# Performance work log

Hardware: AMD Instinct MI355X
Metric: run time of the kernel (lower is better)

## Reference

```python
import jax, jax.numpy as jnp
import numpy as np

N, E, H, L, G = 50000, 800000, 128, 4, 64

def setup_inputs() -> dict:
    key = jax.random.key(0)
    ks = jax.random.split(key, 16)
    s = 0.05
    x = jax.random.normal(ks[0], (N, H), jnp.float32)
    edge_index = jax.random.randint(ks[1], (2, E), 0, N)
    edge_attr = jax.random.normal(ks[2], (E, 1), jnp.float32)
    # sorted graph assignment covering all G graphs (batch[-1]+1 == G)
    batch = (jnp.arange(N) * G) // N
    conv_W1 = jax.random.normal(ks[3], (L, H, H), jnp.float32) * s
    conv_b1 = jnp.zeros((L, H), jnp.float32)
    conv_W2 = jax.random.normal(ks[4], (L, H, H), jnp.float32) * s
    conv_b2 = jnp.zeros((L, H), jnp.float32)
    conv_eps = jnp.zeros((L,), jnp.float32)  # torch init: eps = 0
    edge_W = jax.random.normal(ks[5], (L, 1, H), jnp.float32) * s
    edge_b = jnp.zeros((L, H), jnp.float32)
    vn_W1 = jax.random.normal(ks[6], (L - 1, H, H), jnp.float32) * s
    vn_b1 = jnp.zeros((L - 1, H), jnp.float32)
    vn_W2 = jax.random.normal(ks[7], (L - 1, H, H), jnp.float32) * s
    vn_b2 = jnp.zeros((L - 1, H), jnp.float32)
    vn_emb = jnp.zeros((H,), jnp.float32)  # torch init: constant 0
    return dict(x=x, edge_attr=edge_attr, conv_W1=conv_W1, conv_b1=conv_b1,
                conv_W2=conv_W2, conv_b2=conv_b2, conv_eps=conv_eps,
                edge_W=edge_W, edge_b=edge_b, vn_W1=vn_W1, vn_b1=vn_b1,
                vn_W2=vn_W2, vn_b2=vn_b2, vn_emb=vn_emb,
                edge_index=edge_index, batch=batch)


def reference(x, edge_attr, conv_W1, conv_b1, conv_W2, conv_b2, conv_eps,
              edge_W, edge_b, vn_W1, vn_b1, vn_W2, vn_b2, vn_emb,
              edge_index, batch):
    src, tgt = edge_index[0], edge_index[1]
    # PyG mean aggregation: divide scatter-sum by in-degree (clamped to 1)
    deg = jnp.maximum(
        jax.ops.segment_sum(jnp.ones((E,), x.dtype), tgt, num_segments=N), 1.0)[:, None]
    vn = jnp.broadcast_to(vn_emb[None, :], (G, H))  # virtual node per graph
    h = x
    hs = []
    for i in range(L):
        h = h + vn[batch]
        edge_emb = edge_attr @ edge_W[i] + edge_b[i]          # [E,H]
        msg = jax.nn.relu(h[src] + edge_emb)                   # gather + relu
        agg = jax.ops.segment_sum(msg, tgt, num_segments=N) / deg  # mean scatter
        z = (1.0 + conv_eps[i]) * h + agg
        h = jax.nn.relu(z @ conv_W1[i] + conv_b1[i]) @ conv_W2[i] + conv_b2[i]
        hs.append(h)
        if i < L - 1:
            vt = jax.ops.segment_sum(hs[i], batch, num_segments=G) + vn
            vn = jax.nn.relu(
                jax.nn.relu(vt @ vn_W1[i] + vn_b1[i]) @ vn_W2[i] + vn_b2[i])
            # eval mode: dropout is identity
    return jnp.concatenate(hs, axis=1)  # [N, L*H] jumping-knowledge concat
```

## Files before the change

### kernel.cpp

```cpp
#include <hip/hip_runtime.h>

#define NN 50000
#define EE 800000
#define HH 128
#define LL 4
#define GG 64
#define NR 50048

typedef short bf16x8 __attribute__((ext_vector_type(8)));
typedef float f32x4 __attribute__((ext_vector_type(4)));

__device__ __forceinline__ unsigned bf_round(float f) {
  unsigned u = __float_as_uint(f);
  return (u + 0x7fffu + ((u >> 16) & 1u)) >> 16;
}
__device__ __forceinline__ unsigned bf_pack2(float lo, float hi) {
  return bf_round(lo) | (bf_round(hi) << 16);
}

__global__ __launch_bounds__(256) void count_kernel(const int* __restrict__ tgt,
                                                    int* __restrict__ cnt, int E) {
  int e = blockIdx.x * 256 + threadIdx.x;
  if (e < E) atomicAdd(&cnt[tgt[e]], 1);
}

__global__ __launch_bounds__(256) void blocksum_kernel(const int* __restrict__ cnt,
                                                       int* __restrict__ bs, int N) {
  int i = blockIdx.x * 256 + threadIdx.x;
  int v = (i < N) ? cnt[i] : 0;
  __shared__ int sm[256];
  sm[threadIdx.x] = v;
  __syncthreads();
  for (int s = 128; s >= 1; s >>= 1) {
    if (threadIdx.x < s) sm[threadIdx.x] += sm[threadIdx.x + s];
    __syncthreads();
  }
  if (threadIdx.x == 0) bs[blockIdx.x] = sm[0];
}

__global__ __launch_bounds__(256) void bs_scan_kernel(int* __restrict__ bs, int nb) {
  __shared__ int sm[256];
  int t = threadIdx.x;
  int v = (t < nb) ? bs[t] : 0;
  sm[t] = v;
  __syncthreads();
  for (int off = 1; off < 256; off <<= 1) {
    int u = (t >= off) ? sm[t - off] : 0;
    __syncthreads();
    sm[t] += u;
    __syncthreads();
  }
  if (t < nb) bs[t] = sm[t] - v;
  if (t == 255) bs[nb] = sm[255];
}

__global__ __launch_bounds__(256) void blockscan_kernel(const int* __restrict__ cnt,
                                                        const int* __restrict__ bs,
                                                        int* __restrict__ rp,
                                                        int* __restrict__ cur, int N, int nb) {
  int b = blockIdx.x, t = threadIdx.x;
  int i = b * 256 + t;
  int v = (i < N) ? cnt[i] : 0;
  __shared__ int sm[256];
  sm[t] = v;
  __syncthreads();
  for (int off = 1; off < 256; off <<= 1) {
    int u = (t >= off) ? sm[t - off] : 0;
    __syncthreads();
    sm[t] += u;
    __syncthreads();
  }
  if (i < N) { rp[i] = sm[t] - v + bs[b]; cur[i] = 0; }
  if (b == 0 && t == 0) rp[N] = bs[nb];
}

__global__ __launch_bounds__(256) void scatter_kernel(const int* __restrict__ src,
                                                      const int* __restrict__ tgt,
                                                      const float* __restrict__ attr,
                                                      const int* __restrict__ rp,
                                                      int* __restrict__ cur,
                                                      int2* __restrict__ es, int E) {
  int e = blockIdx.x * 256 + threadIdx.x;
  if (e < E) {
    int t = tgt[e];
    int p = rp[t] + atomicAdd(&cur[t], 1);
    int2 rec;
    rec.x = src[e];
    rec.y = __float_as_int(attr[e]);
    es[p] = rec;
  }
}

__global__ __launch_bounds__(256) void init_kernel(const float* __restrict__ W1,
                                                   const float* __restrict__ W2,
                                                   const float* __restrict__ emb,
                                                   short* __restrict__ wt1,
                                                   short* __restrict__ wt2,
                                                   float* __restrict__ vn,
                                                   float* __restrict__ part) {
  int idx = blockIdx.x * 256 + threadIdx.x;
  const int NW = 2 * LL * HH * HH;
  if (idx < NW) {
    int m = idx >> 14;
    int r = idx & 16383;
    int n = r >> 7, k = r & 127;
    const float* W = (m < LL) ? (W1 + (size_t)m * 16384) : (W2 + (size_t)(m - LL) * 16384);
    short* D = (m < LL) ? (wt1 + (size_t)m * 16384) : (wt2 + (size_t)(m - LL) * 16384);
    D[n * 128 + k] = (short)bf_round(W[k * 128 + n]);
  } else if (idx < NW + GG * HH) {
    int i = idx - NW;
    vn[i] = emb[i & (HH - 1)];
  } else if (idx < NW + 2 * GG * HH) {
    part[idx - NW - GG * HH] = 0.f;
  }
}

__global__ __launch_bounds__(256) void pack_kernel(const float4* __restrict__ hp, int pitch4,
                                                   const float4* __restrict__ vn,
                                                   const float4* __restrict__ ebias,
                                                   const int* __restrict__ batch,
                                                   uint2* __restrict__ hbf, int N) {
  int idx = blockIdx.x * 256 + threadIdx.x;
  if (idx >= N * (HH / 4)) return;
  int n = idx >> 5;
  int c4 = idx & 31;
  int g = batch[n];
  float4 a = hp[(size_t)n * pitch4 + c4];
  float4 b = vn[g * 32 + c4];
  float4 e = ebias[c4];
  uint2 o;
  o.x = bf_pack2(a.x + b.x + e.x, a.y + b.y + e.y);
  o.y = bf_pack2(a.z + b.z + e.z, a.w + b.w + e.w);
  hbf[idx] = o;
}

__device__ __forceinline__ void accum8s(float* acc, uint4 p, float a, float m,
                                        const float4& ew0, const float4& ew1) {
  acc[0] = fmaf(m, fmaxf(fmaf(a, ew0.x, __uint_as_float(p.x << 16)), 0.f), acc[0]);
  acc[1] = fmaf(m, fmaxf(fmaf(a, ew0.y, __uint_as_float(p.x & 0xffff0000u)), 0.f), acc[1]);
  acc[2] = fmaf(m, fmaxf(fmaf(a, ew0.z, __uint_as_float(p.y << 16)), 0.f), acc[2]);
  acc[3] = fmaf(m, fmaxf(fmaf(a, ew0.w, __uint_as_float(p.y & 0xffff0000u)), 0.f), acc[3]);
  acc[4] = fmaf(m, fmaxf(fmaf(a, ew1.x, __uint_as_float(p.z << 16)), 0.f), acc[4]);
  acc[5] = fmaf(m, fmaxf(fmaf(a, ew1.y, __uint_as_float(p.z & 0xffff0000u)), 0.f), acc[5]);
  acc[6] = fmaf(m, fmaxf(fmaf(a, ew1.z, __uint_as_float(p.w << 16)), 0.f), acc[6]);
  acc[7] = fmaf(m, fmaxf(fmaf(a, ew1.w, __uint_as_float(p.w & 0xffff0000u)), 0.f), acc[7]);
}

__global__ __launch_bounds__(128) void agg_kernel(const uint4* __restrict__ hbf4,
                                                  const float* __restrict__ hp, int pitch,
                                                  const float* __restrict__ vnp,
                                                  const int* __restrict__ batch,
                                                  const int2* __restrict__ es,
                                                  const int* __restrict__ rp,
                                                  const float* __restrict__ eW,
                                                  const float* __restrict__ epsp,
                                                  uint4* __restrict__ zb4, int N) {
  int wave = threadIdx.x >> 6;
  int lane = threadIdx.x & 63;
  int n = blockIdx.x * 2 + wave;
  if (n >= N) return;
  int q = lane >> 4;
  int c = lane & 15;
  float4 ew0 = *(const float4*)(eW + c * 8);
  float4 ew1 = *(const float4*)(eW + c * 8 + 4);
  int rs = rp[n], re = rp[n + 1];
  int cnt = re - rs;
  float acc[8];
#pragma unroll
  for (int j = 0; j < 8; ++j) acc[j] = 0.f;
  for (int k = 0; k < cnt; k += 16) {
    int i0 = rs + min(k + q, cnt - 1);
    int i1 = rs + min(k + 4 + q, cnt - 1);
    int i2 = rs + min(k + 8 + q, cnt - 1);
    int i3 = rs + min(k + 12 + q, cnt - 1);
    int2 e0 = es[i0];
    int2 e1 = es[i1];
    int2 e2 = es[i2];
    int2 e3 = es[i3];
    uint4 p0 = hbf4[(size_t)e0.x * 16 + c];
    uint4 p1 = hbf4[(size_t)e1.x * 16 + c];
    uint4 p2 = hbf4[(size_t)e2.x * 16 + c];
    uint4 p3 = hbf4[(size_t)e3.x * 16 + c];
    float m0 = (k + q < cnt) ? 1.f : 0.f;
    float m1 = (k + 4 + q < cnt) ? 1.f : 0.f;
    float m2 = (k + 8 + q < cnt) ? 1.f : 0.f;
    float m3 = (k + 12 + q < cnt) ? 1.f : 0.f;
    accum8s(acc, p0, __int_as_float(e0.y), m0, ew0, ew1);
    accum8s(acc, p1, __int_as_float(e1.y), m1, ew0, ew1);
    accum8s(acc, p2, __int_as_float(e2.y), m2, ew0, ew1);
    accum8s(acc, p3, __int_as_float(e3.y), m3, ew0, ew1);
  }
#pragma unroll
  for (int j = 0; j < 8; ++j) {
    acc[j] += __shfl_xor(acc[j], 16);
    acc[j] += __shfl_xor(acc[j], 32);
  }
  int g = batch[n];
  const float* hrow = hp + (size_t)n * pitch + c * 8;
  const float* vrow = vnp + g * HH + c * 8;
  float4 h0 = *(const float4*)(hrow);
  float4 h1 = *(const float4*)(hrow + 4);
  float4 v0 = *(const float4*)(vrow);
  float4 v1 = *(const float4*)(vrow + 4);
  float inv = 1.f / fmaxf((float)cnt, 1.f);
  float onep = 1.f + epsp[0];
  uint4 o;
  o.x = bf_pack2(fmaf(onep, h0.x + v0.x, acc[0] * inv),
                 fmaf(onep, h0.y + v0.y, acc[1] * inv));
  o.y = bf_pack2(fmaf(onep, h0.z + v0.z, acc[2] * inv),
                 fmaf(onep, h0.w + v0.w, acc[3] * inv));
  o.z = bf_pack2(fmaf(onep, h1.x + v1.x, acc[4] * inv),
                 fmaf(onep, h1.y + v1.y, acc[5] * inv));
  o.w = bf_pack2(fmaf(onep, h1.z + v1.z, acc[6] * inv),
                 fmaf(onep, h1.w + v1.w, acc[7] * inv));
  if (q == 0) zb4[(size_t)n * 16 + c] = o;
}

__global__ __launch_bounds__(256) void mlp_kernel(const unsigned* __restrict__ zb,
                                                  const short* __restrict__ wt1,
                                                  const float* __restrict__ b1,
                                                  const short* __restrict__ wt2,
                                                  const float* __restrict__ b2,
                                                  float* __restrict__ out,
                                                  float* __restrict__ part,
                                                  int do_gs, int layer, int N) {
  __shared__ char smem[64 * 272];
  int tid = threadIdx.x;
  int w = tid >> 6, lane = tid & 63;
  int l15 = lane & 15, q = lane >> 4;
  int row0 = blockIdx.x * 64;
  int wrow = w * 16;

  const uint4* z4 = (const uint4*)zb;
#pragma unroll
  for (int it = 0; it < 4; ++it) {
    int f = lane + it * 64;
    int r = f >> 4, c16 = f & 15;
    uint4 v = z4[(size_t)(row0 + wrow + r) * 16 + c16];
    *(uint4*)(&smem[(wrow + r) * 272 + c16 * 16]) = v;
  }

  f32x4 zero = {0.f, 0.f, 0.f, 0.f};
  f32x4 acc[8];
#pragma unroll
  for (int j = 0; j < 8; ++j) acc[j] = zero;

#pragma unroll
  for (int s = 0; s < 4; ++s) {
    bf16x8 af = *(const bf16x8*)(&smem[(wrow + l15) * 272 + (s * 32 + q * 8) * 2]);
#pragma unroll
    for (int j = 0; j < 8; ++j) {
      bf16x8 bf = *(const bf16x8*)(wt1 + (size_t)(j * 16 + l15) * 128 + s * 32 + q * 8);
      acc[j] = __builtin_amdgcn_mfma_f32_16x16x32_bf16(af, bf, acc[j], 0, 0, 0);
    }
  }
#pragma unroll
  for (int j = 0; j < 8; ++j) {
    float bv = b1[j * 16 + l15];
#pragma unroll
    for (int r = 0; r < 4; ++r) {
      float v = fmaxf(acc[j][r] + bv, 0.f);
      *(short*)(&smem[(wrow + q * 4 + r) * 272 + (j * 16 + l15) * 2]) = (short)bf_round(v);
    }
    acc[j] = zero;
  }
#pragma unroll
  for (int s = 0; s < 4; ++s) {
    bf16x8 af = *(const bf16x8*)(&smem[(wrow + l15) * 272 + (s * 32 + q * 8) * 2]);
#pragma unroll
    for (int j = 0; j < 8; ++j) {
      bf16x8 bf = *(const bf16x8*)(wt2 + (size_t)(j * 16 + l15) * 128 + s * 32 + q * 8);
      acc[j] = __builtin_amdgcn_mfma_f32_16x16x32_bf16(af, bf, acc[j], 0, 0, 0);
    }
  }
  int g0 = (int)(((long long)row0 * GG) / NN);
#pragma unroll
  for (int j = 0; j < 8; ++j) {
    float bv = b2[j * 16 + l15];
    float s0 = 0.f, s1 = 0.f;
#pragma unroll
    for (int r = 0; r < 4; ++r) {
      int row = row0 + wrow + q * 4 + r;
      if (row < N) {
        float v = acc[j][r] + bv;
        out[(size_t)row * (LL * HH) + layer * HH + j * 16 + l15] = v;
        if (do_gs) {
          int rel = (int)(((long long)row * GG) / NN) - g0;
          if (rel == 0) s0 += v; else s1 += v;
        }
      }
    }
    if (do_gs) {
      s0 += __shfl_xor(s0, 16); s0 += __shfl_xor(s0, 32);
      s1 += __shfl_xor(s1, 16); s1 += __shfl_xor(s1, 32);
      if (q == 0) {
        atomicAdd(&part[g0 * HH + j * 16 + l15], s0);
        if (s1 != 0.f) atomicAdd(&part[(g0 + 1) * HH + j * 16 + l15], s1);
      }
    }
  }
}

__global__ __launch_bounds__(128) void vn_fused_kernel(float* __restrict__ part,
                                                       const float* __restrict__ W1,
                                                       const float* __restrict__ b1,
                                                       const float* __restrict__ W2,
                                                       const float* __restrict__ b2,
                                                       float* __restrict__ vn, int G) {
  int g = blockIdx.x, j = threadIdx.x;
  __shared__ float vr[128];
  __shared__ float tr[128];
  vr[j] = vn[g * HH + j] + part[g * HH + j];
  part[g * HH + j] = 0.f;
  __syncthreads();
  float a = b1[j];
  for (int k = 0; k < 128; ++k) a = fmaf(vr[k], W1[k * HH + j], a);
  tr[j] = fmaxf(a, 0.f);
  __syncthreads();
  float o = b2[j];
  for (int k = 0; k < 128; ++k) o = fmaf(tr[k], W2[k * HH + j], o);
  vn[g * HH + j] = fmaxf(o, 0.f);
}

extern "C" void kernel_launch(void* const* d_in, const int* in_sizes, int n_in,
                              void* d_out, int out_size, void* d_ws, size_t ws_size,
                              hipStream_t stream) {
  const int N = NN, E = EE, H = HH, L = LL, G = GG;
  const float* x          = (const float*)d_in[0];
  const float* edge_attr  = (const float*)d_in[1];
  const float* conv_W1    = (const float*)d_in[2];
  const float* conv_b1    = (const float*)d_in[3];
  const float* conv_W2    = (const float*)d_in[4];
  const float* conv_b2    = (const float*)d_in[5];
  const float* conv_eps   = (const float*)d_in[6];
  const float* edge_W     = (const float*)d_in[7];
  const float* edge_b     = (const float*)d_in[8];
  const float* vn_W1      = (const float*)d_in[9];
  const float* vn_b1      = (const float*)d_in[10];
  const float* vn_W2      = (const float*)d_in[11];
  const float* vn_b2      = (const float*)d_in[12];
  const float* vn_emb     = (const float*)d_in[13];
  const int*   edge_index = (const int*)d_in[14];
  const int*   batch      = (const int*)d_in[15];
  float* out = (float*)d_out;

  const int nb = (N + 255) / 256;

  char* ws = (char*)d_ws;
  size_t off = 0;
  auto take = [&](size_t bytes) -> void* {
    void* p = ws + off;
    off = (off + bytes + 255) & ~(size_t)255;
    return p;
  };
  int*      cnt  = (int*)take((size_t)N * 4);
  int*      cur  = (int*)take((size_t)N * 4);
  int*      rp   = (int*)take((size_t)(N + 1) * 4);
  int*      bs   = (int*)take((size_t)(nb + 1) * 4);
  int2*     es   = (int2*)take((size_t)E * 8);
  unsigned* hbf  = (unsigned*)take((size_t)N * (H / 2) * 4);
  unsigned* zb   = (unsigned*)take((size_t)NR * (H / 2) * 4);
  short*    wt1  = (short*)take((size_t)L * H * H * 2);
  short*    wt2  = (short*)take((size_t)L * H * H * 2);
  float*    part = (float*)take((size_t)G * H * 4);
  float*    vn   = (float*)take((size_t)G * H * 4);

  const int* src = edge_index;
  const int* tgt = edge_index + E;

  hipMemsetAsync(cnt, 0, (size_t)N * 4, stream);
  count_kernel<<<(E + 255) / 256, 256, 0, stream>>>(tgt, cnt, E);
  blocksum_kernel<<<nb, 256, 0, stream>>>(cnt, bs, N);
  bs_scan_kernel<<<1, 256, 0, stream>>>(bs, nb);
  blockscan_kernel<<<nb, 256, 0, stream>>>(cnt, bs, rp, cur, N, nb);
  scatter_kernel<<<(E + 255) / 256, 256, 0, stream>>>(src, tgt, edge_attr, rp, cur, es, E);
  init_kernel<<<(2 * L * H * H + 2 * G * H + 255) / 256, 256, 0, stream>>>(
      conv_W1, conv_W2, vn_emb, wt1, wt2, vn, part);

  for (int i = 0; i < L; ++i) {
    const float* hp;
    int pitch;
    if (i == 0) { hp = x; pitch = H; }
    else        { hp = out + (size_t)(i - 1) * H; pitch = L * H; }
    pack_kernel<<<(N * (H / 4) + 255) / 256, 256, 0, stream>>>(
        (const float4*)hp, pitch / 4, (const float4*)vn,
        (const float4*)(edge_b + (size_t)i * H), batch, (uint2*)hbf, N);
    agg_kernel<<<(N + 1) / 2, 128, 0, stream>>>(
        (const uint4*)hbf, hp, pitch, vn, batch, es, rp,
        edge_W + (size_t)i * H, conv_eps + i, (uint4*)zb, N);
    mlp_kernel<<<NR / 64, 256, 0, stream>>>(
        zb, wt1 + (size_t)i * H * H, conv_b1 + (size_t)i * H,
        wt2 + (size_t)i * H * H, conv_b2 + (size_t)i * H, out, part,
        (i < L - 1) ? 1 : 0, i, N);
    if (i < L - 1) {
      vn_fused_kernel<<<G, 128, 0, stream>>>(part, vn_W1 + (size_t)i * H * H,
                                             vn_b1 + (size_t)i * H,
                                             vn_W2 + (size_t)i * H * H,
                                             vn_b2 + (size_t)i * H, vn, G);
    }
  }
}
```

Before: 625.6 us.

## Fuse neighbor aggregation into the MLP kernel via shared memory

Merges the per-node gather/mean aggregation kernel into the MLP kernel. Each wave now aggregates its 16 rows one after another and writes the bf16 z rows straight into shared memory, replacing the global zb buffer. This removes a kernel launch and the global write and re-read of z. The cost is far fewer waves in flight for the latency-bound gather (one wave handles 16 nodes serially instead of one node per wave), which may hurt memory-latency hiding.

```diff
diff --git a/kernel.cpp b/kernel.cpp
--- a/kernel.cpp
+++ b/kernel.cpp
@@ -146,84 +146,21 @@
   acc[7] = fmaf(m, fmaxf(fmaf(a, ew1.w, __uint_as_float(p.w & 0xffff0000u)), 0.f), acc[7]);
 }
 
-__global__ __launch_bounds__(128) void agg_kernel(const uint4* __restrict__ hbf4,
-                                                  const float* __restrict__ hp, int pitch,
-                                                  const float* __restrict__ vnp,
-                                                  const int* __restrict__ batch,
-                                                  const int2* __restrict__ es,
-                                                  const int* __restrict__ rp,
-                                                  const float* __restrict__ eW,
-                                                  const float* __restrict__ epsp,
-                                                  uint4* __restrict__ zb4, int N) {
-  int wave = threadIdx.x >> 6;
-  int lane = threadIdx.x & 63;
-  int n = blockIdx.x * 2 + wave;
-  if (n >= N) return;
-  int q = lane >> 4;
-  int c = lane & 15;
-  float4 ew0 = *(const float4*)(eW + c * 8);
-  float4 ew1 = *(const float4*)(eW + c * 8 + 4);
-  int rs = rp[n], re = rp[n + 1];
-  int cnt = re - rs;
-  float acc[8];
-#pragma unroll
-  for (int j = 0; j < 8; ++j) acc[j] = 0.f;
-  for (int k = 0; k < cnt; k += 16) {
-    int i0 = rs + min(k + q, cnt - 1);
-    int i1 = rs + min(k + 4 + q, cnt - 1);
-    int i2 = rs + min(k + 8 + q, cnt - 1);
-    int i3 = rs + min(k + 12 + q, cnt - 1);
-    int2 e0 = es[i0];
-    int2 e1 = es[i1];
-    int2 e2 = es[i2];
-    int2 e3 = es[i3];
-    uint4 p0 = hbf4[(size_t)e0.x * 16 + c];
-    uint4 p1 = hbf4[(size_t)e1.x * 16 + c];
-    uint4 p2 = hbf4[(size_t)e2.x * 16 + c];
-    uint4 p3 = hbf4[(size_t)e3.x * 16 + c];
-    float m0 = (k + q < cnt) ? 1.f : 0.f;
-    float m1 = (k + 4 + q < cnt) ? 1.f : 0.f;
-    float m2 = (k + 8 + q < cnt) ? 1.f : 0.f;
-    float m3 = (k + 12 + q < cnt) ? 1.f : 0.f;
-    accum8s(acc, p0, __int_as_float(e0.y), m0, ew0, ew1);
-    accum8s(acc, p1, __int_as_float(e1.y), m1, ew0, ew1);
-    accum8s(acc, p2, __int_as_float(e2.y), m2, ew0, ew1);
-    accum8s(acc, p3, __int_as_float(e3.y), m3, ew0, ew1);
-  }
-#pragma unroll
-  for (int j = 0; j < 8; ++j) {
-    acc[j] += __shfl_xor(acc[j], 16);
-    acc[j] += __shfl_xor(acc[j], 32);
-  }
-  int g = batch[n];
-  const float* hrow = hp + (size_t)n * pitch + c * 8;
-  const float* vrow = vnp + g * HH + c * 8;
-  float4 h0 = *(const float4*)(hrow);
-  float4 h1 = *(const float4*)(hrow + 4);
-  float4 v0 = *(const float4*)(vrow);
-  float4 v1 = *(const float4*)(vrow + 4);
-  float inv = 1.f / fmaxf((float)cnt, 1.f);
-  float onep = 1.f + epsp[0];
-  uint4 o;
-  o.x = bf_pack2(fmaf(onep, h0.x + v0.x, acc[0] * inv),
-                 fmaf(onep, h0.y + v0.y, acc[1] * inv));
-  o.y = bf_pack2(fmaf(onep, h0.z + v0.z, acc[2] * inv),
-                 fmaf(onep, h0.w + v0.w, acc[3] * inv));
-  o.z = bf_pack2(fmaf(onep, h1.x + v1.x, acc[4] * inv),
-                 fmaf(onep, h1.y + v1.y, acc[5] * inv));
-  o.w = bf_pack2(fmaf(onep, h1.z + v1.z, acc[6] * inv),
-                 fmaf(onep, h1.w + v1.w, acc[7] * inv));
-  if (q == 0) zb4[(size_t)n * 16 + c] = o;
-}
-
-__global__ __launch_bounds__(256) void mlp_kernel(const unsigned* __restrict__ zb,
-                                                  const short* __restrict__ wt1,
-                                                  const float* __restrict__ b1,
-                                                  const short* __restrict__ wt2,
-                                                  const float* __restrict__ b2,
-                                                  float* __restrict__ out,
-                                                  float* __restrict__ part,
-                                                  int do_gs, int layer, int N) {
+__global__ __launch_bounds__(256) void aggmlp_kernel(const uint4* __restrict__ hbf4,
+                                                     const float* __restrict__ hp, int pitch,
+                                                     const float* __restrict__ vnp,
+                                                     const int* __restrict__ batch,
+                                                     const int2* __restrict__ es,
+                                                     const int* __restrict__ rp,
+                                                     const float* __restrict__ eW,
+                                                     const float* __restrict__ epsp,
+                                                     const short* __restrict__ wt1,
+                                                     const float* __restrict__ b1,
+                                                     const short* __restrict__ wt2,
+                                                     const float* __restrict__ b2,
+                                                     float* __restrict__ out,
+                                                     float* __restrict__ part,
+                                                     int do_gs, int layer, int N) {
   __shared__ char smem[64 * 272];
   int tid = threadIdx.x;
   int w = tid >> 6, lane = tid & 63;
@@ -231,13 +168,65 @@
   int row0 = blockIdx.x * 64;
   int wrow = w * 16;
 
-  const uint4* z4 = (const uint4*)zb;
-#pragma unroll
-  for (int it = 0; it < 4; ++it) {
-    int f = lane + it * 64;
-    int r = f >> 4, c16 = f & 15;
-    uint4 v = z4[(size_t)(row0 + wrow + r) * 16 + c16];
-    *(uint4*)(&smem[(wrow + r) * 272 + c16 * 16]) = v;
+  {
+    int c = l15;
+    float4 ew0 = *(const float4*)(eW + c * 8);
+    float4 ew1 = *(const float4*)(eW + c * 8 + 4);
+    float onep = 1.f + epsp[0];
+    for (int r = 0; r < 16; ++r) {
+      int n = row0 + wrow + r;
+      if (n >= N) break;
+      int rs = rp[n], re = rp[n + 1];
+      int cnt = re - rs;
+      float acc[8];
+#pragma unroll
+      for (int j = 0; j < 8; ++j) acc[j] = 0.f;
+      for (int k = 0; k < cnt; k += 16) {
+        int i0 = rs + min(k + q, cnt - 1);
+        int i1 = rs + min(k + 4 + q, cnt - 1);
+        int i2 = rs + min(k + 8 + q, cnt - 1);
+        int i3 = rs + min(k + 12 + q, cnt - 1);
+        int2 e0 = es[i0];
+        int2 e1 = es[i1];
+        int2 e2 = es[i2];
+        int2 e3 = es[i3];
+        uint4 p0 = hbf4[(size_t)e0.x * 16 + c];
+        uint4 p1 = hbf4[(size_t)e1.x * 16 + c];
+        uint4 p2 = hbf4[(size_t)e2.x * 16 + c];
+        uint4 p3 = hbf4[(size_t)e3.x * 16 + c];
+        float m0 = (k + q < cnt) ? 1.f : 0.f;
+        float m1 = (k + 4 + q < cnt) ? 1.f : 0.f;
+        float m2 = (k + 8 + q < cnt) ? 1.f : 0.f;
+        float m3 = (k + 12 + q < cnt) ? 1.f : 0.f;
+        accum8s(acc, p0, __int_as_float(e0.y), m0, ew0, ew1);
+        accum8s(acc, p1, __int_as_float(e1.y), m1, ew0, ew1);
+        accum8s(acc, p2, __int_as_float(e2.y), m2, ew0, ew1);
+        accum8s(acc, p3, __int_as_float(e3.y), m3, ew0, ew1);
+      }
+#pragma unroll
+      for (int j = 0; j < 8; ++j) {
+        acc[j] += __shfl_xor(acc[j], 16);
+        acc[j] += __shfl_xor(acc[j], 32);
+      }
+      int g = batch[n];
+      const float* hrow = hp + (size_t)n * pitch + c * 8;
+      const float* vrow = vnp + (size_t)g * HH + c * 8;
+      float4 h0 = *(const float4*)(hrow);
+      float4 h1 = *(const float4*)(hrow + 4);
+      float4 v0 = *(const float4*)(vrow);
+      float4 v1 = *(const float4*)(vrow + 4);
+      float inv = 1.f / fmaxf((float)cnt, 1.f);
+      uint4 o;
+      o.x = bf_pack2(fmaf(onep, h0.x + v0.x, acc[0] * inv),
+                     fmaf(onep, h0.y + v0.y, acc[1] * inv));
+      o.y = bf_pack2(fmaf(onep, h0.z + v0.z, acc[2] * inv),
+                     fmaf(onep, h0.w + v0.w, acc[3] * inv));
+      o.z = bf_pack2(fmaf(onep, h1.x + v1.x, acc[4] * inv),
+                     fmaf(onep, h1.y + v1.y, acc[5] * inv));
+      o.w = bf_pack2(fmaf(onep, h1.z + v1.z, acc[6] * inv),
+                     fmaf(onep, h1.w + v1.w, acc[7] * inv));
+      if (q == 0) *(uint4*)(&smem[(wrow + r) * 272 + c * 16]) = o;
+    }
   }
 
   f32x4 zero = {0.f, 0.f, 0.f, 0.f};
@@ -359,7 +348,6 @@
   int*      bs   = (int*)take((size_t)(nb + 1) * 4);
   int2*     es   = (int2*)take((size_t)E * 8);
   unsigned* hbf  = (unsigned*)take((size_t)N * (H / 2) * 4);
-  unsigned* zb   = (unsigned*)take((size_t)NR * (H / 2) * 4);
   short*    wt1  = (short*)take((size_t)L * H * H * 2);
   short*    wt2  = (short*)take((size_t)L * H * H * 2);
   float*    part = (float*)take((size_t)G * H * 4);
@@ -385,11 +373,10 @@
     pack_kernel<<<(N * (H / 4) + 255) / 256, 256, 0, stream>>>(
         (const float4*)hp, pitch / 4, (const float4*)vn,
         (const float4*)(edge_b + (size_t)i * H), batch, (uint2*)hbf, N);
-    agg_kernel<<<(N + 1) / 2, 128, 0, stream>>>(
+    aggmlp_kernel<<<NR / 64, 256, 0, stream>>>(
         (const uint4*)hbf, hp, pitch, vn, batch, es, rp,
-        edge_W + (size_t)i * H, conv_eps + i, (uint4*)zb, N);
-    mlp_kernel<<<NR / 64, 256, 0, stream>>>(
-        zb, wt1 + (size_t)i * H * H, conv_b1 + (size_t)i * H,
+        edge_W + (size_t)i * H, conv_eps + i,
+        wt1 + (size_t)i * H * H, conv_b1 + (size_t)i * H,
         wt2 + (size_t)i * H * H, conv_b2 + (size_t)i * H, out, part,
         (i < L - 1) ? 1 : 0, i, N);
     if (i < L - 1) {
```

New measurement: 758.6 us. +21.3%, slower.

## Fuse bf16 packing into MLP epilogue and add virtual node during aggregation

Applied to the files above, without the earlier changes.

Removes the per-layer pack kernel. The MLP kernel now writes the next layer's bf16 gather buffer (h plus the next edge bias) directly in its epilogue, and the aggregation kernel adds the per-graph virtual node vector on the fly. It gets the graph id from batch[src], packed into the upper bits of the edge record. The count and init kernels are merged into one launch. This saves a full N×H read/write pass per layer plus some launches, at the cost of extra vn loads (L2-resident) per gathered edge and 2-byte scattered stores in the MLP epilogue. Packing src into 16 bits relies on N < 65536.

```diff
diff --git a/kernel.cpp b/kernel.cpp
--- a/kernel.cpp
+++ b/kernel.cpp
@@ -18,10 +18,35 @@
   return bf_round(lo) | (bf_round(hi) << 16);
 }
 
-__global__ __launch_bounds__(256) void count_kernel(const int* __restrict__ tgt,
-                                                    int* __restrict__ cnt, int E) {
-  int e = blockIdx.x * 256 + threadIdx.x;
-  if (e < E) atomicAdd(&cnt[tgt[e]], 1);
+__global__ __launch_bounds__(256) void count_init_kernel(const int* __restrict__ tgt,
+                                                         int* __restrict__ cnt, int E, int nbE,
+                                                         const float* __restrict__ W1,
+                                                         const float* __restrict__ W2,
+                                                         const float* __restrict__ emb,
+                                                         short* __restrict__ wt1,
+                                                         short* __restrict__ wt2,
+                                                         float* __restrict__ vn,
+                                                         float* __restrict__ part) {
+  if ((int)blockIdx.x < nbE) {
+    int e = blockIdx.x * 256 + threadIdx.x;
+    if (e < E) atomicAdd(&cnt[tgt[e]], 1);
+    return;
+  }
+  int idx = (blockIdx.x - nbE) * 256 + threadIdx.x;
+  const int NW = 2 * LL * HH * HH;
+  if (idx < NW) {
+    int m = idx >> 14;
+    int r = idx & 16383;
+    int n = r >> 7, k = r & 127;
+    const float* W = (m < LL) ? (W1 + (size_t)m * 16384) : (W2 + (size_t)(m - LL) * 16384);
+    short* D = (m < LL) ? (wt1 + (size_t)m * 16384) : (wt2 + (size_t)(m - LL) * 16384);
+    D[n * 128 + k] = (short)bf_round(W[k * 128 + n]);
+  } else if (idx < NW + GG * HH) {
+    int i = idx - NW;
+    vn[i] = emb[i & (HH - 1)];
+  } else if (idx < NW + 2 * GG * HH) {
+    part[idx - NW - GG * HH] = 0.f;
+  }
 }
 
 __global__ __launch_bounds__(256) void blocksum_kernel(const int* __restrict__ cnt,
@@ -79,71 +104,50 @@
                                                       const float* __restrict__ attr,
                                                       const int* __restrict__ rp,
                                                       int* __restrict__ cur,
+                                                      const int* __restrict__ batch,
                                                       int2* __restrict__ es, int E) {
   int e = blockIdx.x * 256 + threadIdx.x;
   if (e < E) {
     int t = tgt[e];
+    int s = src[e];
     int p = rp[t] + atomicAdd(&cur[t], 1);
     int2 rec;
-    rec.x = src[e];
+    rec.x = s | (batch[s] << 16);
     rec.y = __float_as_int(attr[e]);
     es[p] = rec;
   }
 }
 
-__global__ __launch_bounds__(256) void init_kernel(const float* __restrict__ W1,
-                                                   const float* __restrict__ W2,
-                                                   const float* __restrict__ emb,
-                                                   short* __restrict__ wt1,
-                                                   short* __restrict__ wt2,
-                                                   float* __restrict__ vn,
-                                                   float* __restrict__ part) {
-  int idx = blockIdx.x * 256 + threadIdx.x;
-  const int NW = 2 * LL * HH * HH;
-  if (idx < NW) {
-    int m = idx >> 14;
-    int r = idx & 16383;
-    int n = r >> 7, k = r & 127;
-    const float* W = (m < LL) ? (W1 + (size_t)m * 16384) : (W2 + (size_t)(m - LL) * 16384);
-    short* D = (m < LL) ? (wt1 + (size_t)m * 16384) : (wt2 + (size_t)(m - LL) * 16384);
-    D[n * 128 + k] = (short)bf_round(W[k * 128 + n]);
-  } else if (idx < NW + GG * HH) {
-    int i = idx - NW;
-    vn[i] = emb[i & (HH - 1)];
-  } else if (idx < NW + 2 * GG * HH) {
-    part[idx - NW - GG * HH] = 0.f;
-  }
-}
-
-__global__ __launch_bounds__(256) void pack_kernel(const float4* __restrict__ hp, int pitch4,
-                                                   const float4* __restrict__ vn,
-                                                   const float4* __restrict__ ebias,
-                                                   const int* __restrict__ batch,
-                                                   uint2* __restrict__ hbf, int N) {
+__global__ __launch_bounds__(256) void pack0_kernel(const float4* __restrict__ xp,
+                                                    const float4* __restrict__ ebias,
+                                                    uint2* __restrict__ hbf, int N) {
   int idx = blockIdx.x * 256 + threadIdx.x;
   if (idx >= N * (HH / 4)) return;
-  int n = idx >> 5;
   int c4 = idx & 31;
-  int g = batch[n];
-  float4 a = hp[(size_t)n * pitch4 + c4];
-  float4 b = vn[g * 32 + c4];
+  float4 a = xp[idx];
   float4 e = ebias[c4];
   uint2 o;
-  o.x = bf_pack2(a.x + b.x + e.x, a.y + b.y + e.y);
-  o.y = bf_pack2(a.z + b.z + e.z, a.w + b.w + e.w);
+  o.x = bf_pack2(a.x + e.x, a.y + e.y);
+  o.y = bf_pack2(a.z + e.z, a.w + e.w);
   hbf[idx] = o;
 }
 
-__device__ __forceinline__ void accum8s(float* acc, uint4 p, float a, float m,
+__device__ __forceinline__ void accum8v(float* acc, uint4 p, float a, float m,
+                                        const float4& va, const float4& vb,
                                         const float4& ew0, const float4& ew1) {
-  acc[0] = fmaf(m, fmaxf(fmaf(a, ew0.x, __uint_as_float(p.x << 16)), 0.f), acc[0]);
-  acc[1] = fmaf(m, fmaxf(fmaf(a, ew0.y, __uint_as_float(p.x & 0xffff0000u)), 0.f), acc[1]);
-  acc[2] = fmaf(m, fmaxf(fmaf(a, ew0.z, __uint_as_float(p.y << 16)), 0.f), acc[2]);
-  acc[3] = fmaf(m, fmaxf(fmaf(a, ew0.w, __uint_as_float(p.y & 0xffff0000u)), 0.f), acc[3]);
-  acc[4] = fmaf(m, fmaxf(fmaf(a, ew1.x, __uint_as_float(p.z << 16)), 0.f), acc[4]);
-  acc[5] = fmaf(m, fmaxf(fmaf(a, ew1.y, __uint_as_float(p.z & 0xffff0000u)), 0.f), acc[5]);
-  acc[6] = fmaf(m, fmaxf(fmaf(a, ew1.z, __uint_as_float(p.w << 16)), 0.f), acc[6]);
-  acc[7] = fmaf(m, fmaxf(fmaf(a, ew1.w, __uint_as_float(p.w & 0xffff0000u)), 0.f), acc[7]);
+  float lo, hi;
+  lo = __uint_as_float(p.x << 16); hi = __uint_as_float(p.x & 0xffff0000u);
+  acc[0] = fmaf(m, fmaxf(fmaf(a, ew0.x, lo + va.x), 0.f), acc[0]);
+  acc[1] = fmaf(m, fmaxf(fmaf(a, ew0.y, hi + va.y), 0.f), acc[1]);
+  lo = __uint_as_float(p.y << 16); hi = __uint_as_float(p.y & 0xffff0000u);
+  acc[2] = fmaf(m, fmaxf(fmaf(a, ew0.z, lo + va.z), 0.f), acc[2]);
+  acc[3] = fmaf(m, fmaxf(fmaf(a, ew0.w, hi + va.w), 0.f), acc[3]);
+  lo = __uint_as_float(p.z << 16); hi = __uint_as_float(p.z & 0xffff0000u);
+  acc[4] = fmaf(m, fmaxf(fmaf(a, ew1.x, lo + vb.x), 0.f), acc[4]);
+  acc[5] = fmaf(m, fmaxf(fmaf(a, ew1.y, hi + vb.y), 0.f), acc[5]);
+  lo = __uint_as_float(p.w << 16); hi = __uint_as_float(p.w & 0xffff0000u);
+  acc[6] = fmaf(m, fmaxf(fmaf(a, ew1.z, lo + vb.z), 0.f), acc[6]);
+  acc[7] = fmaf(m, fmaxf(fmaf(a, ew1.w, hi + vb.w), 0.f), acc[7]);
 }
 
 __global__ __launch_bounds__(128) void agg_kernel(const uint4* __restrict__ hbf4,
@@ -177,18 +181,28 @@
     int2 e1 = es[i1];
     int2 e2 = es[i2];
     int2 e3 = es[i3];
-    uint4 p0 = hbf4[(size_t)e0.x * 16 + c];
-    uint4 p1 = hbf4[(size_t)e1.x * 16 + c];
-    uint4 p2 = hbf4[(size_t)e2.x * 16 + c];
-    uint4 p3 = hbf4[(size_t)e3.x * 16 + c];
+    unsigned x0 = (unsigned)e0.x, x1 = (unsigned)e1.x;
+    unsigned x2 = (unsigned)e2.x, x3 = (unsigned)e3.x;
+    uint4 p0 = hbf4[(size_t)(x0 & 0xffffu) * 16 + c];
+    uint4 p1 = hbf4[(size_t)(x1 & 0xffffu) * 16 + c];
+    uint4 p2 = hbf4[(size_t)(x2 & 0xffffu) * 16 + c];
+    uint4 p3 = hbf4[(size_t)(x3 & 0xffffu) * 16 + c];
+    const float4* vr0 = (const float4*)(vnp + (x0 >> 16) * HH + c * 8);
+    const float4* vr1 = (const float4*)(vnp + (x1 >> 16) * HH + c * 8);
+    const float4* vr2 = (const float4*)(vnp + (x2 >> 16) * HH + c * 8);
+    const float4* vr3 = (const float4*)(vnp + (x3 >> 16) * HH + c * 8);
+    float4 va0 = vr0[0], vb0 = vr0[1];
+    float4 va1 = vr1[0], vb1 = vr1[1];
+    float4 va2 = vr2[0], vb2 = vr2[1];
+    float4 va3 = vr3[0], vb3 = vr3[1];
     float m0 = (k + q < cnt) ? 1.f : 0.f;
     float m1 = (k + 4 + q < cnt) ? 1.f : 0.f;
     float m2 = (k + 8 + q < cnt) ? 1.f : 0.f;
     float m3 = (k + 12 + q < cnt) ? 1.f : 0.f;
-    accum8s(acc, p0, __int_as_float(e0.y), m0, ew0, ew1);
-    accum8s(acc, p1, __int_as_float(e1.y), m1, ew0, ew1);
-    accum8s(acc, p2, __int_as_float(e2.y), m2, ew0, ew1);
-    accum8s(acc, p3, __int_as_float(e3.y), m3, ew0, ew1);
+    accum8v(acc, p0, __int_as_float(e0.y), m0, va0, vb0, ew0, ew1);
+    accum8v(acc, p1, __int_as_float(e1.y), m1, va1, vb1, ew0, ew1);
+    accum8v(acc, p2, __int_as_float(e2.y), m2, va2, vb2, ew0, ew1);
+    accum8v(acc, p3, __int_as_float(e3.y), m3, va3, vb3, ew0, ew1);
   }
 #pragma unroll
   for (int j = 0; j < 8; ++j) {
@@ -223,7 +237,9 @@
                                                   const float* __restrict__ b2,
                                                   float* __restrict__ out,
                                                   float* __restrict__ part,
-                                                  int do_gs, int layer, int N) {
+                                                  short* __restrict__ hbfw,
+                                                  const float* __restrict__ ebn,
+                                                  int do_gs, int do_hbf, int layer, int N) {
   __shared__ char smem[64 * 272];
   int tid = threadIdx.x;
   int w = tid >> 6, lane = tid & 63;
@@ -277,6 +293,7 @@
 #pragma unroll
   for (int j = 0; j < 8; ++j) {
     float bv = b2[j * 16 + l15];
+    float ebv = do_hbf ? ebn[j * 16 + l15] : 0.f;
     float s0 = 0.f, s1 = 0.f;
 #pragma unroll
     for (int r = 0; r < 4; ++r) {
@@ -284,6 +301,8 @@
       if (row < N) {
         float v = acc[j][r] + bv;
         out[(size_t)row * (LL * HH) + layer * HH + j * 16 + l15] = v;
+        if (do_hbf)
+          hbfw[(size_t)row * HH + j * 16 + l15] = (short)bf_round(v + ebv);
         if (do_gs) {
           int rel = (int)(((long long)row * GG) / NN) - g0;
           if (rel == 0) s0 += v; else s1 += v;
@@ -345,6 +364,7 @@
   float* out = (float*)d_out;
 
   const int nb = (N + 255) / 256;
+  const int nbE = (E + 255) / 256;
 
   char* ws = (char*)d_ws;
   size_t off = 0;
@@ -369,29 +389,31 @@
   const int* tgt = edge_index + E;
 
   hipMemsetAsync(cnt, 0, (size_t)N * 4, stream);
-  count_kernel<<<(E + 255) / 256, 256, 0, stream>>>(tgt, cnt, E);
+  const int initBlocks = (2 * L * H * H + 2 * G * H + 255) / 256;
+  count_init_kernel<<<nbE + initBlocks, 256, 0, stream>>>(
+      tgt, cnt, E, nbE, conv_W1, conv_W2, vn_emb, wt1, wt2, vn, part);
   blocksum_kernel<<<nb, 256, 0, stream>>>(cnt, bs, N);
   bs_scan_kernel<<<1, 256, 0, stream>>>(bs, nb);
   blockscan_kernel<<<nb, 256, 0, stream>>>(cnt, bs, rp, cur, N, nb);
-  scatter_kernel<<<(E + 255) / 256, 256, 0, stream>>>(src, tgt, edge_attr, rp, cur, es, E);
-  init_kernel<<<(2 * L * H * H + 2 * G * H + 255) / 256, 256, 0, stream>>>(
-      conv_W1, conv_W2, vn_emb, wt1, wt2, vn, part);
+  scatter_kernel<<<nbE, 256, 0, stream>>>(src, tgt, edge_attr, rp, cur, batch, es, E);
+
+  pack0_kernel<<<(N * (H / 4) + 255) / 256, 256, 0, stream>>>(
+      (const float4*)x, (const float4*)edge_b, (uint2*)hbf, N);
 
   for (int i = 0; i < L; ++i) {
     const float* hp;
     int pitch;
     if (i == 0) { hp = x; pitch = H; }
     else        { hp = out + (size_t)(i - 1) * H; pitch = L * H; }
-    pack_kernel<<<(N * (H / 4) + 255) / 256, 256, 0, stream>>>(
-        (const float4*)hp, pitch / 4, (const float4*)vn,
-        (const float4*)(edge_b + (size_t)i * H), batch, (uint2*)hbf, N);
     agg_kernel<<<(N + 1) / 2, 128, 0, stream>>>(
         (const uint4*)hbf, hp, pitch, vn, batch, es, rp,
         edge_W + (size_t)i * H, conv_eps + i, (uint4*)zb, N);
+    int do_hbf = (i < L - 1) ? 1 : 0;
     mlp_kernel<<<NR / 64, 256, 0, stream>>>(
         zb, wt1 + (size_t)i * H * H, conv_b1 + (size_t)i * H,
         wt2 + (size_t)i * H * H, conv_b2 + (size_t)i * H, out, part,
-        (i < L - 1) ? 1 : 0, i, N);
+        (short*)hbf, edge_b + (size_t)(i + 1) * H,
+        do_hbf, do_hbf, i, N);
     if (i < L - 1) {
       vn_fused_kernel<<<G, 128, 0, stream>>>(part, vn_W1 + (size_t)i * H * H,
                                              vn_b1 + (size_t)i * H,
```

After: 645.2 us. 3.1% more time.

## Fuse setup kernels and merge virtual-node MLP with next-layer bf16 pack

Applied to the files above, without the earlier changes.

Merges the degree count, weight transpose/init and layer-0 pack into one launch, and replaces the three-kernel scan with a single scan kernel in which each block recomputes its own prefix. The per-layer pack kernel is folded into the virtual-node MLP kernel, which now runs 8 blocks per graph that each redo the tiny MLP and pack a slice of that graph's nodes. Ping-pong buffers for vn and part avoid read/write races between blocks. The aim is fewer launches and fewer serialized small kernels, paid for with redundant MLP compute and a quadratic prefix loop in the scan.

```diff
diff --git a/kernel.cpp b/kernel.cpp
--- a/kernel.cpp
+++ b/kernel.cpp
@@ -6,6 +6,7 @@
 #define LL 4
 #define GG 64
 #define NR 50048
+#define NS 8
 
 typedef short bf16x8 __attribute__((ext_vector_type(8)));
 typedef float f32x4 __attribute__((ext_vector_type(4)));
@@ -18,30 +19,67 @@
   return bf_round(lo) | (bf_round(hi) << 16);
 }
 
-__global__ __launch_bounds__(256) void count_kernel(const int* __restrict__ tgt,
-                                                    int* __restrict__ cnt, int E) {
-  int e = blockIdx.x * 256 + threadIdx.x;
-  if (e < E) atomicAdd(&cnt[tgt[e]], 1);
-}
-
-__global__ __launch_bounds__(256) void blocksum_kernel(const int* __restrict__ cnt,
-                                                       int* __restrict__ bs, int N) {
-  int i = blockIdx.x * 256 + threadIdx.x;
+__global__ __launch_bounds__(256) void count_init_pack0_kernel(
+    const int* __restrict__ tgt, int* __restrict__ cnt, int E, int nbE, int initB,
+    const float* __restrict__ W1, const float* __restrict__ W2,
+    const float* __restrict__ emb, short* __restrict__ wt1, short* __restrict__ wt2,
+    float* __restrict__ vnA, float* __restrict__ part01,
+    const float4* __restrict__ x4, const float* __restrict__ eb0,
+    uint2* __restrict__ hbf, int N) {
+  int bid = blockIdx.x;
+  int t = threadIdx.x;
+  if (bid < nbE) {
+    int e = bid * 256 + t;
+    if (e < E) atomicAdd(&cnt[tgt[e]], 1);
+    return;
+  }
+  if (bid < nbE + initB) {
+    int idx = (bid - nbE) * 256 + t;
+    const int NW = 2 * LL * HH * HH;
+    if (idx < NW) {
+      int m = idx >> 14;
+      int r = idx & 16383;
+      int n = r >> 7, k = r & 127;
+      const float* W = (m < LL) ? (W1 + (size_t)m * 16384) : (W2 + (size_t)(m - LL) * 16384);
+      short* D = (m < LL) ? (wt1 + (size_t)m * 16384) : (wt2 + (size_t)(m - LL) * 16384);
+      D[n * 128 + k] = (short)bf_round(W[k * 128 + n]);
+    } else if (idx < NW + GG * HH) {
+      int i = idx - NW;
+      vnA[i] = emb[i & (HH - 1)];
+    } else if (idx < NW + 3 * GG * HH) {
+      part01[idx - NW - GG * HH] = 0.f;
+    }
+    return;
+  }
+  int pidx = (bid - nbE - initB) * 256 + t;
+  if (pidx >= N * (HH / 4)) return;
+  int c4 = pidx & 31;
+  float4 a = x4[pidx];
+  const float4 v = *(const float4*)(emb + c4 * 4);
+  const float4 e = *(const float4*)(eb0 + c4 * 4);
+  uint2 o;
+  o.x = bf_pack2(a.x + v.x + e.x, a.y + v.y + e.y);
+  o.y = bf_pack2(a.z + v.z + e.z, a.w + v.w + e.w);
+  hbf[pidx] = o;
+}
+
+__global__ __launch_bounds__(256) void rp_scan_kernel(const int* __restrict__ cnt,
+                                                      int* __restrict__ rp,
+                                                      int* __restrict__ cur, int N, int nb) {
+  int b = blockIdx.x, t = threadIdx.x;
+  int i = b * 256 + t;
+  int pre = 0;
+  for (int j = t; j < b * 256; j += 256) pre += cnt[j];
+  __shared__ int sm[256];
+  sm[t] = pre;
+  __syncthreads();
+  for (int s = 128; s >= 1; s >>= 1) {
+    if (t < s) sm[t] += sm[t + s];
+    __syncthreads();
+  }
+  int prefix = sm[0];
+  __syncthreads();
   int v = (i < N) ? cnt[i] : 0;
-  __shared__ int sm[256];
-  sm[threadIdx.x] = v;
-  __syncthreads();
-  for (int s = 128; s >= 1; s >>= 1) {
-    if (threadIdx.x < s) sm[threadIdx.x] += sm[threadIdx.x + s];
-    __syncthreads();
-  }
-  if (threadIdx.x == 0) bs[blockIdx.x] = sm[0];
-}
-
-__global__ __launch_bounds__(256) void bs_scan_kernel(int* __restrict__ bs, int nb) {
-  __shared__ int sm[256];
-  int t = threadIdx.x;
-  int v = (t < nb) ? bs[t] : 0;
   sm[t] = v;
   __syncthreads();
   for (int off = 1; off < 256; off <<= 1) {
@@ -50,28 +88,8 @@
     sm[t] += u;
     __syncthreads();
   }
-  if (t < nb) bs[t] = sm[t] - v;
-  if (t == 255) bs[nb] = sm[255];
-}
-
-__global__ __launch_bounds__(256) void blockscan_kernel(const int* __restrict__ cnt,
-                                                        const int* __restrict__ bs,
-                                                        int* __restrict__ rp,
-                                                        int* __restrict__ cur, int N, int nb) {
-  int b = blockIdx.x, t = threadIdx.x;
-  int i = b * 256 + t;
-  int v = (i < N) ? cnt[i] : 0;
-  __shared__ int sm[256];
-  sm[t] = v;
-  __syncthreads();
-  for (int off = 1; off < 256; off <<= 1) {
-    int u = (t >= off) ? sm[t - off] : 0;
-    __syncthreads();
-    sm[t] += u;
-    __syncthreads();
-  }
-  if (i < N) { rp[i] = sm[t] - v + bs[b]; cur[i] = 0; }
-  if (b == 0 && t == 0) rp[N] = bs[nb];
+  if (i < N) { rp[i] = prefix + sm[t] - v; cur[i] = 0; }
+  if (b == nb - 1 && t == 255) rp[N] = prefix + sm[255];
 }
 
 __global__ __launch_bounds__(256) void scatter_kernel(const int* __restrict__ src,
@@ -89,49 +107,6 @@
     rec.y = __float_as_int(attr[e]);
     es[p] = rec;
   }
-}
-
-__global__ __launch_bounds__(256) void init_kernel(const float* __restrict__ W1,
-                                                   const float* __restrict__ W2,
-                                                   const float* __restrict__ emb,
-                                                   short* __restrict__ wt1,
-                                                   short* __restrict__ wt2,
-                                                   float* __restrict__ vn,
-                                                   float* __restrict__ part) {
-  int idx = blockIdx.x * 256 + threadIdx.x;
-  const int NW = 2 * LL * HH * HH;
-  if (idx < NW) {
-    int m = idx >> 14;
-    int r = idx & 16383;
-    int n = r >> 7, k = r & 127;
-    const float* W = (m < LL) ? (W1 + (size_t)m * 16384) : (W2 + (size_t)(m - LL) * 16384);
-    short* D = (m < LL) ? (wt1 + (size_t)m * 16384) : (wt2 + (size_t)(m - LL) * 16384);
-    D[n * 128 + k] = (short)bf_round(W[k * 128 + n]);
-  } else if (idx < NW + GG * HH) {
-    int i = idx - NW;
-    vn[i] = emb[i & (HH - 1)];
-  } else if (idx < NW + 2 * GG * HH) {
-    part[idx - NW - GG * HH] = 0.f;
-  }
-}
-
-__global__ __launch_bounds__(256) void pack_kernel(const float4* __restrict__ hp, int pitch4,
-                                                   const float4* __restrict__ vn,
-                                                   const float4* __restrict__ ebias,
-                                                   const int* __restrict__ batch,
-                                                   uint2* __restrict__ hbf, int N) {
-  int idx = blockIdx.x * 256 + threadIdx.x;
-  if (idx >= N * (HH / 4)) return;
-  int n = idx >> 5;
-  int c4 = idx & 31;
-  int g = batch[n];
-  float4 a = hp[(size_t)n * pitch4 + c4];
-  float4 b = vn[g * 32 + c4];
-  float4 e = ebias[c4];
-  uint2 o;
-  o.x = bf_pack2(a.x + b.x + e.x, a.y + b.y + e.y);
-  o.y = bf_pack2(a.z + b.z + e.z, a.w + b.w + e.w);
-  hbf[idx] = o;
 }
 
 __device__ __forceinline__ void accum8s(float* acc, uint4 p, float a, float m,
@@ -301,25 +276,61 @@
   }
 }
 
-__global__ __launch_bounds__(128) void vn_fused_kernel(float* __restrict__ part,
-                                                       const float* __restrict__ W1,
-                                                       const float* __restrict__ b1,
-                                                       const float* __restrict__ W2,
-                                                       const float* __restrict__ b2,
-                                                       float* __restrict__ vn, int G) {
-  int g = blockIdx.x, j = threadIdx.x;
+__global__ __launch_bounds__(256) void vnpack_kernel(const float* __restrict__ part_in,
+                                                     float* __restrict__ part_zero,
+                                                     const float* __restrict__ vn_in,
+                                                     float* __restrict__ vn_out,
+                                                     const float* __restrict__ W1,
+                                                     const float* __restrict__ b1,
+                                                     const float* __restrict__ W2,
+                                                     const float* __restrict__ b2,
+                                                     const float* __restrict__ outp,
+                                                     const float* __restrict__ ebn,
+                                                     uint2* __restrict__ hbf,
+                                                     int layer, int N) {
+  int b = blockIdx.x;
+  int g = b >> 3, s = b & (NS - 1);
+  int t = threadIdx.x;
   __shared__ float vr[128];
   __shared__ float tr[128];
-  vr[j] = vn[g * HH + j] + part[g * HH + j];
-  part[g * HH + j] = 0.f;
-  __syncthreads();
-  float a = b1[j];
-  for (int k = 0; k < 128; ++k) a = fmaf(vr[k], W1[k * HH + j], a);
-  tr[j] = fmaxf(a, 0.f);
-  __syncthreads();
-  float o = b2[j];
-  for (int k = 0; k < 128; ++k) o = fmaf(tr[k], W2[k * HH + j], o);
-  vn[g * HH + j] = fmaxf(o, 0.f);
+  __shared__ float vo[128];
+  if (t < 128) vr[t] = vn_in[g * HH + t] + part_in[g * HH + t];
+  __syncthreads();
+  if (t < 128) {
+    float a = b1[t];
+    for (int k = 0; k < 128; ++k) a = fmaf(vr[k], W1[k * HH + t], a);
+    tr[t] = fmaxf(a, 0.f);
+  }
+  __syncthreads();
+  if (t < 128) {
+    float o = b2[t];
+    for (int k = 0; k < 128; ++k) o = fmaf(tr[k], W2[k * HH + t], o);
+    float vn = fmaxf(o, 0.f);
+    vo[t] = vn;
+    if (s == 0) {
+      vn_out[g * HH + t] = vn;
+      part_zero[g * HH + t] = 0.f;
+    }
+  }
+  __syncthreads();
+  int r0 = (g * NN + GG - 1) / GG;
+  int r1 = ((g + 1) * NN + GG - 1) / GG;
+  if (r1 > N) r1 = N;
+  int len = r1 - r0;
+  int chunk = (len + NS - 1) / NS;
+  int rs = r0 + s * chunk;
+  int re = min(rs + chunk, r1);
+  int c4 = t & 31;
+  float4 v = *(const float4*)(vo + c4 * 4);
+  float4 e = *(const float4*)(ebn + c4 * 4);
+  const float4* o4 = (const float4*)outp;
+  for (int n = rs + (t >> 5); n < re; n += 8) {
+    float4 a = o4[(size_t)n * (LL * HH / 4) + layer * (HH / 4) + c4];
+    uint2 o;
+    o.x = bf_pack2(a.x + v.x + e.x, a.y + v.y + e.y);
+    o.y = bf_pack2(a.z + v.z + e.z, a.w + v.w + e.w);
+    hbf[(size_t)n * 32 + c4] = o;
+  }
 }
 
 extern "C" void kernel_launch(void* const* d_in, const int* in_sizes, int n_in,
@@ -345,6 +356,7 @@
   float* out = (float*)d_out;
 
   const int nb = (N + 255) / 256;
+  const int nbE = (E + 255) / 256;
 
   char* ws = (char*)d_ws;
   size_t off = 0;
@@ -353,50 +365,53 @@
     off = (off + bytes + 255) & ~(size_t)255;
     return p;
   };
-  int*      cnt  = (int*)take((size_t)N * 4);
-  int*      cur  = (int*)take((size_t)N * 4);
-  int*      rp   = (int*)take((size_t)(N + 1) * 4);
-  int*      bs   = (int*)take((size_t)(nb + 1) * 4);
-  int2*     es   = (int2*)take((size_t)E * 8);
-  unsigned* hbf  = (unsigned*)take((size_t)N * (H / 2) * 4);
-  unsigned* zb   = (unsigned*)take((size_t)NR * (H / 2) * 4);
-  short*    wt1  = (short*)take((size_t)L * H * H * 2);
-  short*    wt2  = (short*)take((size_t)L * H * H * 2);
-  float*    part = (float*)take((size_t)G * H * 4);
-  float*    vn   = (float*)take((size_t)G * H * 4);
+  int*      cnt   = (int*)take((size_t)N * 4);
+  int*      cur   = (int*)take((size_t)N * 4);
+  int*      rp    = (int*)take((size_t)(N + 1) * 4);
+  int2*     es    = (int2*)take((size_t)E * 8);
+  unsigned* hbf   = (unsigned*)take((size_t)N * (H / 2) * 4);
+  unsigned* zb    = (unsigned*)take((size_t)NR * (H / 2) * 4);
+  short*    wt1   = (short*)take((size_t)L * H * H * 2);
+  short*    wt2   = (short*)take((size_t)L * H * H * 2);
+  float*    part  = (float*)take((size_t)2 * G * H * 4);
+  float*    vnA   = (float*)take((size_t)G * H * 4);
+  float*    vnB   = (float*)take((size_t)G * H * 4);
 
   const int* src = edge_index;
   const int* tgt = edge_index + E;
 
   hipMemsetAsync(cnt, 0, (size_t)N * 4, stream);
-  count_kernel<<<(E + 255) / 256, 256, 0, stream>>>(tgt, cnt, E);
-  blocksum_kernel<<<nb, 256, 0, stream>>>(cnt, bs, N);
-  bs_scan_kernel<<<1, 256, 0, stream>>>(bs, nb);
-  blockscan_kernel<<<nb, 256, 0, stream>>>(cnt, bs, rp, cur, N, nb);
-  scatter_kernel<<<(E + 255) / 256, 256, 0, stream>>>(src, tgt, edge_attr, rp, cur, es, E);
-  init_kernel<<<(2 * L * H * H + 2 * G * H + 255) / 256, 256, 0, stream>>>(
-      conv_W1, conv_W2, vn_emb, wt1, wt2, vn, part);
+  const int initB = (2 * L * H * H + 3 * G * H + 255) / 256;
+  const int packB = (N * (H / 4) + 255) / 256;
+  count_init_pack0_kernel<<<nbE + initB + packB, 256, 0, stream>>>(
+      tgt, cnt, E, nbE, initB, conv_W1, conv_W2, vn_emb, wt1, wt2, vnA, part,
+      (const float4*)x, edge_b, (uint2*)hbf, N);
+  rp_scan_kernel<<<nb, 256, 0, stream>>>(cnt, rp, cur, N, nb);
+  scatter_kernel<<<nbE, 256, 0, stream>>>(src, tgt, edge_attr, rp, cur, es, E);
 
   for (int i = 0; i < L; ++i) {
     const float* hp;
     int pitch;
     if (i == 0) { hp = x; pitch = H; }
     else        { hp = out + (size_t)(i - 1) * H; pitch = L * H; }
-    pack_kernel<<<(N * (H / 4) + 255) / 256, 256, 0, stream>>>(
-        (const float4*)hp, pitch / 4, (const float4*)vn,
-        (const float4*)(edge_b + (size_t)i * H), batch, (uint2*)hbf, N);
+    float* vin  = (i & 1) ? vnB : vnA;
+    float* vout = (i & 1) ? vnA : vnB;
     agg_kernel<<<(N + 1) / 2, 128, 0, stream>>>(
-        (const uint4*)hbf, hp, pitch, vn, batch, es, rp,
+        (const uint4*)hbf, hp, pitch, vin, batch, es, rp,
         edge_W + (size_t)i * H, conv_eps + i, (uint4*)zb, N);
     mlp_kernel<<<NR / 64, 256, 0, stream>>>(
         zb, wt1 + (size_t)i * H * H, conv_b1 + (size_t)i * H,
-        wt2 + (size_t)i * H * H, conv_b2 + (size_t)i * H, out, part,
+        wt2 + (size_t)i * H * H, conv_b2 + (size_t)i * H, out,
+        part + (size_t)(i & 1) * G * H,
         (i < L - 1) ? 1 : 0, i, N);
     if (i < L - 1) {
-      vn_fused_kernel<<<G, 128, 0, stream>>>(part, vn_W1 + (size_t)i * H * H,
-                                             vn_b1 + (size_t)i * H,
-                                             vn_W2 + (size_t)i * H * H,
-                                             vn_b2 + (size_t)i * H, vn, G);
-    }
-  }
-}
+      vnpack_kernel<<<G * NS, 256, 0, stream>>>(
+          part + (size_t)(i & 1) * G * H,
+          part + (size_t)((i + 1) & 1) * G * H,
+          vin, vout,
+          vn_W1 + (size_t)i * H * H, vn_b1 + (size_t)i * H,
+          vn_W2 + (size_t)i * H * H, vn_b2 + (size_t)i * H,
+          out, edge_b + (size_t)(i + 1) * H, (uint2*)hbf, i, N);
+    }
+  }
+}
```

Result: no change. 621.5 us (-0.7%).
